# Kernel optimization log

Measured on AMD Instinct MI355X. Metric: run time of the kernel, lower is better.

Reference implementation:

```python
import jax, jax.numpy as jnp
import numpy as np

B, C, H, W = 32, 256, 64, 64
K = 3  # kernel taps along channel axis
BN_EPS = 1e-5


def setup_inputs() -> dict:
    key = jax.random.key(0)
    ks = jax.random.split(key, 6)
    x = jax.random.normal(ks[0], (B, C, H, W), dtype=jnp.float32)
    # 1x1 conv weight: Conv2d(C, K*C, 1, bias=False) -> [K*C, C]
    conv_w = jax.random.normal(ks[1], (K * C, C), dtype=jnp.float32) * (1.0 / np.sqrt(C))
    # BatchNorm2d(K*C) in eval mode: weight, bias, running stats
    bn_w = jax.random.uniform(ks[2], (K * C,), dtype=jnp.float32, minval=0.5, maxval=1.5)
    bn_b = jax.random.normal(ks[3], (K * C,), dtype=jnp.float32) * 0.1
    bn_mean = jax.random.normal(ks[4], (K * C,), dtype=jnp.float32) * 0.1
    bn_var = jax.random.uniform(ks[5], (K * C,), dtype=jnp.float32, minval=0.5, maxval=1.5)
    # affine residual params (original init: gamma=0, beta=1; use small random gamma
    # so the dynamic-filter branch contributes to the output / gradients)
    gamma = jax.random.normal(jax.random.fold_in(key, 7), (C, 1, 1), dtype=jnp.float32) * 0.1
    beta = jnp.ones((C, 1, 1), dtype=jnp.float32)
    return {"x": x, "conv_w": conv_w, "bn_w": bn_w, "bn_b": bn_b,
            "bn_mean": bn_mean, "bn_var": bn_var, "gamma": gamma, "beta": beta}


def reference(x, conv_w, bn_w, bn_b, bn_mean, bn_var, gamma, beta):
    b, c, h, w = x.shape
    # GAP -> 1x1 conv -> BN(eval) -> sigmoid : per-(sample, tap, channel) filter
    gap = x.mean(axis=(2, 3))                                # [B, C]
    f = jnp.einsum('bc,oc->bo', gap, conv_w)                 # [B, K*C]
    f = (f - bn_mean) * jax.lax.rsqrt(bn_var + BN_EPS) * bn_w + bn_b
    filt = jax.nn.sigmoid(f).reshape(b, K, c)                # [B, K, C]
    # dynamic 3-tap conv along the channel axis with reflect padding
    xp = jnp.pad(x, ((0, 0), (1, 1), (0, 0), (0, 0)), mode='reflect')  # [B, C+2, H, W]
    out = filt[:, 0, :, None, None] * xp[:, 0:c]
    for k in range(1, K):
        out = out + filt[:, k, :, None, None] * xp[:, k:k + c]
    # affine residual fuse
    return out * gamma + x * beta
```

## Files before the change

kernel.cpp:

```cpp
#include <hip/hip_runtime.h>
#include <math.h>

#define Bn   32
#define Cn   256
#define Kn   3
#define HWn  4096
#define HW4n 1024
#define BN_EPS 1e-5f
#define SPC  16
#define NSTRIP (Cn / SPC)

typedef float f4 __attribute__((ext_vector_type(4)));

__global__ __launch_bounds__(256) void gap_kernel(const float* __restrict__ x,
                                                  float* __restrict__ gap) {
    const int bc = blockIdx.x;
    const f4* px = (const f4*)(x + (size_t)bc * HWn);
    const int t = threadIdx.x;
    float s = 0.f;
#pragma unroll
    for (int i = 0; i < 4; ++i) {
        f4 v = px[t + i * 256];
        s += (v.x + v.y) + (v.z + v.w);
    }
#pragma unroll
    for (int off = 32; off > 0; off >>= 1) s += __shfl_down(s, off, 64);
    __shared__ float ls[4];
    const int wave = t >> 6, lane = t & 63;
    if (lane == 0) ls[wave] = s;
    __syncthreads();
    if (t == 0) {
        gap[bc] = (ls[0] + ls[1] + ls[2] + ls[3]) * (1.0f / (float)HWn);
    }
}

__global__ __launch_bounds__(256) void stencil_kernel(
        const float* __restrict__ x, const float* __restrict__ gap,
        const float* __restrict__ conv_w,
        const float* __restrict__ bn_w, const float* __restrict__ bn_b,
        const float* __restrict__ bn_mean, const float* __restrict__ bn_var,
        const float* __restrict__ gamma, const float* __restrict__ beta,
        float* __restrict__ out) {
    const int blk   = blockIdx.x;
    const int half  = blk & 1;
    const int strip = (blk >> 1) & (NSTRIP - 1);
    const int b     = blk >> 5;
    const int c0    = strip * SPC;
    const int t     = threadIdx.x;

    const f4* px = (const f4*)x;
    const size_t base0 = (size_t)b * Cn * HW4n + (size_t)half * 512 + t;
    const size_t base1 = base0 + 256;
    const int cm = (c0 == 0) ? 1 : c0 - 1;
    f4 xm0 = px[base0 + (size_t)cm * HW4n];
    f4 xm1 = px[base1 + (size_t)cm * HW4n];
    f4 xc0 = px[base0 + (size_t)c0 * HW4n];
    f4 xc1 = px[base1 + (size_t)c0 * HW4n];

    __shared__ __align__(16) float gap_s[Cn];
    __shared__ float a0s[SPC], a1s[SPC], a2s[SPC];
    gap_s[t] = gap[b * Cn + t];
    __syncthreads();
    if (t < 192) {
        const int ol = t >> 2, p = t & 3;
        const int k = ol >> 4, cc = ol & 15;
        const int c = c0 + cc;
        const int o = k * Cn + c;
        const f4* w4 = (const f4*)(conv_w + (size_t)o * Cn) + p * 16;
        const f4* g4 = ((const f4*)gap_s) + p * 16;
        float acc = 0.f;
#pragma unroll
        for (int i = 0; i < 16; ++i) {
            f4 g = g4[i], w = w4[i];
            acc += g.x * w.x + g.y * w.y + g.z * w.z + g.w * w.w;
        }
        acc += __shfl_down(acc, 2, 4);
        acc += __shfl_down(acc, 1, 4);
        if (p == 0) {
            float fv = (acc - bn_mean[o]) * rsqrtf(bn_var[o] + BN_EPS) * bn_w[o] + bn_b[o];
            float sg = 1.0f / (1.0f + expf(-fv));
            float a  = (k == 1) ? (sg * gamma[c] + beta[c]) : (sg * gamma[c]);
            if (k == 0) a0s[cc] = a; else if (k == 1) a1s[cc] = a; else a2s[cc] = a;
        }
    }
    __syncthreads();

    f4* pout = (f4*)out;
#pragma unroll 4
    for (int i = 0; i < SPC; ++i) {
        const int c   = c0 + i;
        const int cnn = (c == Cn - 1) ? (Cn - 2) : (c + 1);
        f4 xn0 = px[base0 + (size_t)cnn * HW4n];
        f4 xn1 = px[base1 + (size_t)cnn * HW4n];
        const float a0 = a0s[i], a1 = a1s[i], a2 = a2s[i];
        f4 o0, o1;
        o0.x = fmaf(a0, xm0.x, fmaf(a1, xc0.x, a2 * xn0.x));
        o0.y = fmaf(a0, xm0.y, fmaf(a1, xc0.y, a2 * xn0.y));
        o0.z = fmaf(a0, xm0.z, fmaf(a1, xc0.z, a2 * xn0.z));
        o0.w = fmaf(a0, xm0.w, fmaf(a1, xc0.w, a2 * xn0.w));
        o1.x = fmaf(a0, xm1.x, fmaf(a1, xc1.x, a2 * xn1.x));
        o1.y = fmaf(a0, xm1.y, fmaf(a1, xc1.y, a2 * xn1.y));
        o1.z = fmaf(a0, xm1.z, fmaf(a1, xc1.z, a2 * xn1.z));
        o1.w = fmaf(a0, xm1.w, fmaf(a1, xc1.w, a2 * xn1.w));
        __builtin_nontemporal_store(o0, &pout[base0 + (size_t)c * HW4n]);
        __builtin_nontemporal_store(o1, &pout[base1 + (size_t)c * HW4n]);
        xm0 = xc0; xc0 = xn0;
        xm1 = xc1; xc1 = xn1;
    }
}

extern "C" void kernel_launch(void* const* d_in, const int* in_sizes, int n_in,
                              void* d_out, int out_size, void* d_ws, size_t ws_size,
                              hipStream_t stream) {
    const float* x       = (const float*)d_in[0];
    const float* conv_w  = (const float*)d_in[1];
    const float* bn_w    = (const float*)d_in[2];
    const float* bn_b    = (const float*)d_in[3];
    const float* bn_mean = (const float*)d_in[4];
    const float* bn_var  = (const float*)d_in[5];
    const float* gamma   = (const float*)d_in[6];
    const float* beta    = (const float*)d_in[7];
    float* out = (float*)d_out;

    float* gap = (float*)d_ws;

    gap_kernel<<<Bn * Cn, 256, 0, stream>>>(x, gap);
    stencil_kernel<<<(Bn * NSTRIP * 2), 256, 0, stream>>>(
        x, gap, conv_w, bn_w, bn_b, bn_mean, bn_var, gamma, beta, out);
}
```

Measured before the change: 264.0 us.

## Fuse GAP into stencil kernel with atomic accumulation and per-batch spin barrier

Removes the separate GAP kernel. Each stencil block sums its own 16-channel by half-spatial tile and atomically adds the partial means into a zeroed workspace. A per-batch counter then acts as a spin barrier, so blocks wait until all 32 blocks of their sample have contributed before computing filters. The aim is to cut one launch and to load x into cache just before the stencil reuses it. The cost is a memset, float atomics that make the summation order nondeterministic, and a spin-wait that can deadlock if blocks of one batch are not all co-resident (1024 blocks are launched).

```diff
diff --git a/kernel.cpp b/kernel.cpp
--- a/kernel.cpp
+++ b/kernel.cpp
@@ -9,38 +9,17 @@
 #define BN_EPS 1e-5f
 #define SPC  16
 #define NSTRIP (Cn / SPC)
+#define BLOCKS_PER_B (NSTRIP*2)
 
 typedef float f4 __attribute__((ext_vector_type(4)));
 
-__global__ __launch_bounds__(256) void gap_kernel(const float* __restrict__ x,
-                                                  float* __restrict__ gap) {
-    const int bc = blockIdx.x;
-    const f4* px = (const f4*)(x + (size_t)bc * HWn);
-    const int t = threadIdx.x;
-    float s = 0.f;
-#pragma unroll
-    for (int i = 0; i < 4; ++i) {
-        f4 v = px[t + i * 256];
-        s += (v.x + v.y) + (v.z + v.w);
-    }
-#pragma unroll
-    for (int off = 32; off > 0; off >>= 1) s += __shfl_down(s, off, 64);
-    __shared__ float ls[4];
-    const int wave = t >> 6, lane = t & 63;
-    if (lane == 0) ls[wave] = s;
-    __syncthreads();
-    if (t == 0) {
-        gap[bc] = (ls[0] + ls[1] + ls[2] + ls[3]) * (1.0f / (float)HWn);
-    }
-}
-
-__global__ __launch_bounds__(256) void stencil_kernel(
-        const float* __restrict__ x, const float* __restrict__ gap,
-        const float* __restrict__ conv_w,
+__global__ __launch_bounds__(256) void fused_kernel(
+        const float* __restrict__ x, const float* __restrict__ conv_w,
         const float* __restrict__ bn_w, const float* __restrict__ bn_b,
         const float* __restrict__ bn_mean, const float* __restrict__ bn_var,
         const float* __restrict__ gamma, const float* __restrict__ beta,
-        float* __restrict__ out) {
+        float* __restrict__ out, float* __restrict__ gap,
+        unsigned int* __restrict__ cnt) {
     const int blk   = blockIdx.x;
     const int half  = blk & 1;
     const int strip = (blk >> 1) & (NSTRIP - 1);
@@ -49,6 +28,34 @@
     const int t     = threadIdx.x;
 
     const f4* px = (const f4*)x;
+
+    {
+        const int ch = t >> 4;
+        const int l  = t & 15;
+        const size_t abase = (size_t)b * Cn * HW4n + (size_t)(c0 + ch) * HW4n
+                           + (size_t)half * 512 + l;
+        float s = 0.f;
+#pragma unroll
+        for (int j = 0; j < 32; ++j) {
+            f4 v = px[abase + (size_t)j * 16];
+            s += (v.x + v.y) + (v.z + v.w);
+        }
+        s += __shfl_down(s, 8, 16);
+        s += __shfl_down(s, 4, 16);
+        s += __shfl_down(s, 2, 16);
+        s += __shfl_down(s, 1, 16);
+        if (l == 0) atomicAdd(&gap[b * Cn + c0 + ch], s * (1.0f / (float)HWn));
+    }
+    __syncthreads();
+    if (t == 0) {
+        __hip_atomic_fetch_add(&cnt[b], 1u, __ATOMIC_RELEASE,
+                               __HIP_MEMORY_SCOPE_AGENT);
+        while (__hip_atomic_load(&cnt[b], __ATOMIC_ACQUIRE,
+                                 __HIP_MEMORY_SCOPE_AGENT) < BLOCKS_PER_B)
+            __builtin_amdgcn_s_sleep(8);
+    }
+    __syncthreads();
+
     const size_t base0 = (size_t)b * Cn * HW4n + (size_t)half * 512 + t;
     const size_t base1 = base0 + 256;
     const int cm = (c0 == 0) ? 1 : c0 - 1;
@@ -122,9 +129,12 @@
     const float* beta    = (const float*)d_in[7];
     float* out = (float*)d_out;
 
-    float* gap = (float*)d_ws;
+    float* gap        = (float*)d_ws;
+    unsigned int* cnt = (unsigned int*)(gap + Bn * Cn);
 
-    gap_kernel<<<Bn * Cn, 256, 0, stream>>>(x, gap);
-    stencil_kernel<<<(Bn * NSTRIP * 2), 256, 0, stream>>>(
-        x, gap, conv_w, bn_w, bn_b, bn_mean, bn_var, gamma, beta, out);
+    hipMemsetAsync(d_ws, 0, Bn * Cn * sizeof(float) + Bn * sizeof(unsigned int),
+                   stream);
+
+    fused_kernel<<<Bn * BLOCKS_PER_B, 256, 0, stream>>>(
+        x, conv_w, bn_w, bn_b, bn_mean, bn_var, gamma, beta, out, gap, cnt);
 }
```

Result: slower. 343.3 us (+30.1%).
